# Kernel optimization log

Measured on AMD Instinct MI355X. Metric: run time of the kernel, lower is better.

The kernel has to match this reference:

```python
import jax, jax.numpy as jnp
import numpy as np

T_STEPS, B, I, H = 512, 64, 128, 256
LAST_K, RSIZE = 16, 32


def _xavier(key, shape):
    fan_out, fan_in = shape[0], shape[-1]
    std = (2.0 / (fan_in + fan_out)) ** 0.5
    return (std * jax.random.normal(key, shape)).astype(jnp.float32)


def setup_inputs() -> dict:
    key = jax.random.key(0)
    ks = jax.random.split(key, 8)
    inp = {"x": jax.random.normal(ks[0], (T_STEPS, B, I), dtype=jnp.float32)}
    for n, k in zip(["Wf", "Wi", "Wo", "Wg"], ks[1:5]):
        inp[n + "_w"] = _xavier(k, (H, H + I))
        inp[n + "_b"] = jnp.zeros((H,), jnp.float32)
    inp["Ua_w"] = _xavier(ks[5], (H, H))
    inp["Va_w"] = _xavier(ks[6], (H, H))
    inp["v"] = _xavier(ks[7], (1, H))
    return inp


def _forward(x, Wf_w, Wf_b, Wi_w, Wi_b, Wo_w, Wo_b, Wg_w, Wg_b, Ua_w, Va_w, v):
    T = x.shape[0]
    vv = v[0]  # [H]
    neg_inf = jnp.float32(-jnp.inf)

    def lstm(st, ct, xt):
        inp = jnp.concatenate([st, xt], axis=1)  # [B, H+I], order (hidden, input) as in torch cat((st, x), 1)
        ft = jax.nn.sigmoid(inp @ Wf_w.T + Wf_b)
        it = jax.nn.sigmoid(inp @ Wi_w.T + Wi_b)
        ot = jax.nn.sigmoid(inp @ Wo_w.T + Wo_b)
        gt = jnp.tanh(inp @ Wg_w.T + Wg_b)
        ct = ft * ct + it * gt
        return ot * jnp.tanh(ct), ct

    # ---- step 0 (reset path): st = zero hidden, no attention ----
    st0 = jnp.zeros((B, H), jnp.float32)
    h0, ct0 = lstm(st0, jnp.zeros((B, H), jnp.float32), x[0])
    mem0 = jnp.zeros((LAST_K, B, H), jnp.float32).at[-1].set(h0)  # ring of last_k hiddens (zeros = not yet filled)
    carry0 = (st0, ct0, mem0,
              jnp.zeros((RSIZE, B, H), jnp.float32),   # long_mem buckets
              jnp.full((RSIZE, B), neg_inf),            # long_mask (-inf = empty bucket)
              jnp.zeros((T, B), jnp.float32),           # long_scores (detached accumulator)
              jnp.zeros((B, RSIZE), jnp.float32),       # buck_scores
              jnp.zeros((B,), jnp.int32))               # per-sample bucket fill count

    def body(carry, tx):
        st, ct, mem, long_mem, long_mask, long_scores, buck, fill = carry
        t, xt = tx
        slots = jnp.arange(LAST_K)
        short_valid = slots >= (LAST_K - t)  # slot j holds h_{t-LAST_K+j}; valid iff time >= 0
        # ---- additive attention over short memory + long-term buckets ----
        q = st @ Va_w.T                              # [B,H]
        Uahs = mem @ Ua_w.T                          # [LAST_K,B,H]
        long_uas = long_mem @ Ua_w.T                 # [RSIZE,B,H]
        es = jnp.einsum('kbh,h->kb', jnp.tanh(q[None] + Uahs), vv)
        es = jnp.where(short_valid[:, None], es, neg_inf)
        es_long = jnp.einsum('rbh,h->rb', jnp.tanh(q[None] + long_uas), vv) + long_mask
        alphas = jax.nn.softmax(jnp.concatenate([es, es_long], 0), axis=0)  # [LAST_K+RSIZE,B]
        # accumulate detached attention mass onto absolute-time scores
        det_a = jax.lax.stop_gradient(alphas[:LAST_K])
        times = jnp.clip(t - LAST_K + slots, 0, T - 1)
        long_scores = long_scores.at[times].add(jnp.where(short_valid[:, None], det_a, 0.0))
        comb = jnp.concatenate([mem, long_mem], 0)   # [LAST_K+RSIZE,B,H]
        ct_att = jnp.einsum('nb,nbh->bh', alphas, comb)
        st = 0.5 * (mem[-1] + ct_att)                # comb_hs[-1-rsize] == previous hidden
        # ---- LSTM gating ----
        hidden, ct = lstm(st, ct, xt)
        # ---- bucket insert / argmin-replace (active once t >= LAST_K) ----
        cand = mem[0]                                # h_{t-LAST_K} == memory[0]
        cand_score = jax.lax.stop_gradient(
            jax.lax.dynamic_index_in_dim(long_scores, jnp.clip(t - LAST_K, 0, T - 1), 0, keepdims=False))  # [B]
        minp = jnp.argmin(buck, axis=1)              # [B], first-min like torch.argmin
        min_val = jnp.take_along_axis(buck, minp[:, None], axis=1)[:, 0]
        full = fill >= RSIZE
        addpos = jnp.where(full, minp, fill)
        do_upd = (t >= LAST_K) & (jnp.logical_not(full) | (cand_score > min_val))
        onehot = (jnp.arange(RSIZE)[None, :] == addpos[:, None]) & do_upd[:, None]  # [B,RSIZE]
        sel = onehot.T                               # [RSIZE,B]
        long_mem = jnp.where(sel[:, :, None], cand[None], long_mem)
        long_mask = jnp.where(sel, 0.0, long_mask)
        buck = jnp.where(onehot, cand_score[:, None], buck)
        fill = fill + (do_upd & jnp.logical_not(full)).astype(jnp.int32)
        # ---- push hidden into short-memory ring ----
        mem = jnp.concatenate([mem[1:], hidden[None]], 0)
        return (st, ct, mem, long_mem, long_mask, long_scores, buck, fill), hidden

    ts = jnp.arange(1, T)
    _, hs = jax.lax.scan(jax.checkpoint(body), carry0, (ts, x[1:]))
    return jnp.concatenate([h0[None], hs], 0)  # [T,B,H]


def reference(x, Wf_w, Wf_b, Wi_w, Wi_b, Wo_w, Wo_b, Wg_w, Wg_b, Ua_w, Va_w, v):
    return _forward(x, Wf_w, Wf_b, Wi_w, Wi_b, Wo_w, Wo_b, Wg_w, Wg_b, Ua_w, Va_w, v)
```

## Files before the change

kernel.cpp:

```cpp
#include <hip/hip_runtime.h>
#include <hip/hip_fp16.h>

#define T_STEPS 512
#define NB      64
#define NI      128
#define NH      256
#define LK      16
#define RS      32
#define NS      (LK + RS)

#define WP_OFF   0
#define VAP8_OFF 786432
#define UAP8_OFF 917504
#define GX_OFF   5242880
#define WS_NEED  (GX_OFF + (size_t)T_STEPS * NB * NH * 8)

typedef _Float16 half2v __attribute__((ext_vector_type(2)));

#if defined(__has_builtin)
# if __has_builtin(__builtin_amdgcn_make_buffer_rsrc) && \
     __has_builtin(__builtin_amdgcn_raw_buffer_load_b128) && \
     __has_builtin(__builtin_amdgcn_raw_buffer_load_b64)
#  define USE_BUFLD 1
# endif
#endif
#ifndef USE_BUFLD
# define USE_BUFLD 0
#endif

template <typename D, typename S>
__device__ __forceinline__ D bcastv(S s) {
    static_assert(sizeof(D) == sizeof(S), "size mismatch");
    D d; __builtin_memcpy(&d, &s, sizeof(D)); return d;
}

#if USE_BUFLD
#define DECL_RSRC(name, ptr) \
    auto name = __builtin_amdgcn_make_buffer_rsrc((void*)(ptr), (short)0, -1, 0x00020000)
#define LD16(name, ptr, idx) \
    bcastv<uint4>(__builtin_amdgcn_raw_buffer_load_b128(name, (int)((idx) * 16), 0, 1))
#define LD8(name, ptr, idx) \
    bcastv<uint2>(__builtin_amdgcn_raw_buffer_load_b64(name, (int)((idx) * 8), 0, 1))
#else
#define DECL_RSRC(name, ptr) int name = 0; (void)name
#define LD16(name, ptr, idx) ((ptr)[idx])
#define LD8(name, ptr, idx)  ((ptr)[idx])
#endif

__device__ __forceinline__ float hdot(unsigned int w, unsigned int s, float c) {
    return __builtin_amdgcn_fdot2(__builtin_bit_cast(half2v, w),
                                  __builtin_bit_cast(half2v, s), c, false);
}

__device__ __forceinline__ float fsig(float x) {
    return __builtin_amdgcn_rcpf(1.0f + __expf(-x));
}
__device__ __forceinline__ float ftanh(float x) {
    x = fminf(15.0f, fmaxf(-15.0f, x));
    float e = __expf(2.0f * x);
    return (e - 1.0f) * __builtin_amdgcn_rcpf(e + 1.0f);
}

__global__ void prep_weights(const float* __restrict__ Wf, const float* __restrict__ Wi,
                             const float* __restrict__ Wo, const float* __restrict__ Wg,
                             const float* __restrict__ Ua, const float* __restrict__ Va,
                             unsigned char* __restrict__ ws) {
    int e = blockIdx.x * 256 + threadIdx.x;
    if (e < 49152) {
        int h = e & 255, k2 = e >> 8, k = 2 * k2;
        uint4 w; __half2 t;
        t = __floats2half2_rn(Wf[h * 384 + k], Wf[h * 384 + k + 1]); w.x = *(unsigned int*)&t;
        t = __floats2half2_rn(Wi[h * 384 + k], Wi[h * 384 + k + 1]); w.y = *(unsigned int*)&t;
        t = __floats2half2_rn(Wo[h * 384 + k], Wo[h * 384 + k + 1]); w.z = *(unsigned int*)&t;
        t = __floats2half2_rn(Wg[h * 384 + k], Wg[h * 384 + k + 1]); w.w = *(unsigned int*)&t;
        ((uint4*)(ws + WP_OFF))[e] = w;
    } else {
        int e2 = e - 49152;
        const float* S = (e2 < 8192) ? Va : Ua;
        int e3 = e2 & 8191;
        int h = e3 & 255, j = e3 >> 8, k = 8 * j;
        uint4 w; __half2 t;
        t = __floats2half2_rn(S[h * 256 + k + 0], S[h * 256 + k + 1]); w.x = *(unsigned int*)&t;
        t = __floats2half2_rn(S[h * 256 + k + 2], S[h * 256 + k + 3]); w.y = *(unsigned int*)&t;
        t = __floats2half2_rn(S[h * 256 + k + 4], S[h * 256 + k + 5]); w.z = *(unsigned int*)&t;
        t = __floats2half2_rn(S[h * 256 + k + 6], S[h * 256 + k + 7]); w.w = *(unsigned int*)&t;
        ((uint4*)(ws + VAP8_OFF))[e2] = w;
    }
}

__global__ __launch_bounds__(256) void gx_gemm(const float* __restrict__ x,
                                               unsigned char* __restrict__ ws) {
    const int t = blockIdx.x, bg = blockIdx.y, tid = threadIdx.x;
    const uint4* __restrict__ WP = (const uint4*)(ws + WP_OFF);
    uint2* __restrict__ GX = (uint2*)(ws + GX_OFF);
    __shared__ float s_xx[16 * 128];
    const float* xb = x + ((size_t)t * NB + bg * 16) * NI;
#pragma unroll
    for (int r = 0; r < 8; ++r) s_xx[tid + 256 * r] = xb[tid + 256 * r];
    __syncthreads();
    const int h = tid;
    float acc[16][4];
#pragma unroll
    for (int bb = 0; bb < 16; ++bb) { acc[bb][0] = acc[bb][1] = acc[bb][2] = acc[bb][3] = 0.f; }
    for (int k2 = 128; k2 < 192; ++k2) {
        uint4 w = WP[k2 * NH + h];
        float2 wf = __half22float2(*(const __half2*)&w.x);
        float2 wi = __half22float2(*(const __half2*)&w.y);
        float2 wo = __half22float2(*(const __half2*)&w.z);
        float2 wg = __half22float2(*(const __half2*)&w.w);
        int kk = 2 * k2 - 256;
#pragma unroll
        for (int bb = 0; bb < 16; ++bb) {
            float2 xv = *(const float2*)(s_xx + bb * 128 + kk);
            acc[bb][0] += wf.x * xv.x + wf.y * xv.y;
            acc[bb][1] += wi.x * xv.x + wi.y * xv.y;
            acc[bb][2] += wo.x * xv.x + wo.y * xv.y;
            acc[bb][3] += wg.x * xv.x + wg.y * xv.y;
        }
    }
#pragma unroll
    for (int bb = 0; bb < 16; ++bb) {
        __half2 p0 = __floats2half2_rn(acc[bb][0], acc[bb][1]);
        __half2 p1 = __floats2half2_rn(acc[bb][2], acc[bb][3]);
        uint2 u; u.x = *(unsigned int*)&p0; u.y = *(unsigned int*)&p1;
        GX[((size_t)t * NB + bg * 16 + bb) * NH + h] = u;
    }
}

template <int USE_GX>
__global__ __launch_bounds__(1024, 1) void rel_lstm(
    const float* __restrict__ x,
    const float* __restrict__ bf_g, const float* __restrict__ bi_g,
    const float* __restrict__ bo_g, const float* __restrict__ bg_g,
    const float* __restrict__ vv_g,
    unsigned char* __restrict__ ws, float* __restrict__ out) {
    const int tid = threadIdx.x;
    const int b   = blockIdx.x;
    const int wv  = tid >> 6;
    const int ln  = tid & 63;
    const int h16 = (wv << 4) | (ln & 15);
    const int kc  = ln >> 4;

    const uint4* __restrict__ WP   = (const uint4*)(ws + WP_OFF);
    const uint4* __restrict__ VaP8 = (const uint4*)(ws + VAP8_OFF);
    const uint2* __restrict__ GX   = (const uint2*)(ws + GX_OFF);
    DECL_RSRC(rWP, ws + WP_OFF);
    DECL_RSRC(rVU, ws + VAP8_OFF);
    DECL_RSRC(rGX, ws + GX_OFF);

    __shared__ __align__(16) _Float16 s_in_h[NH + NI];
    __shared__ __align__(16) _Float16 s_hid_h[NH];
    __shared__ __align__(16) float s_q[NH];
    __shared__ __align__(16) float s_v[NH];
    __shared__ __align__(16) float s_mem[LK][NH];
    __shared__ __align__(16) float s_memua[LK][NH + 8];
    __shared__ __align__(16) float s_lraw[RS * NH];
    __shared__ __align__(16) float s_lua[RS * NH];
    __shared__ float s_es[NS], s_al[NS];
    __shared__ float s_scores[T_STEPS];
    __shared__ float s_mask[RS], s_buck[RS];
    __shared__ float s_minv;
    __shared__ int s_minp, s_fill, s_upd, s_pos;

    for (int i = tid; i < LK * NH; i += 1024) ((float*)s_mem)[i] = 0.f;
    for (int i = tid; i < LK * (NH + 8); i += 1024) ((float*)s_memua)[i] = 0.f;
    for (int i = tid; i < RS * NH; i += 1024) { s_lraw[i] = 0.f; s_lua[i] = 0.f; }
    if (tid < T_STEPS) s_scores[tid] = 0.f;
    if (tid < NH) s_v[tid] = vv_g[tid];
    if (tid < (NH + NI) / 2) ((unsigned int*)s_in_h)[tid] = 0u;
    if (tid < RS) { s_mask[tid] = -1e30f; s_buck[tid] = 0.f; }
    if (tid == 0) { s_fill = 0; s_upd = 0; s_pos = 0; s_minv = 0.f; s_minp = 0; }
    float bfv = 0.f, biv = 0.f, bov = 0.f, bgv = 0.f;
    if (kc == 0) { bfv = bf_g[h16]; biv = bi_g[h16]; bov = bo_g[h16]; bgv = bg_g[h16]; }
    if (!USE_GX && tid < 64) {
        float2 xv = ((const float2*)(x + (size_t)b * NI))[tid];
        __half2 hx = __floats2half2_rn(xv.x, xv.y);
        ((unsigned int*)s_in_h)[NH / 2 + tid] = *(unsigned int*)&hx;
    }
    float ct = 0.f;
    int base = 0;
    __syncthreads();

    for (int t = 0; t < T_STEPS; ++t) {
        float evA = 0.f, evB = 0.f;
        uint2 gx = {0u, 0u};
        if (USE_GX && kc == 0) gx = LD8(rGX, GX, ((size_t)t * NB + b) * NH + h16);
        if (t > 0) {
            {
                const int pofs = (wv < 8) ? 0 : 8192;
                const uint4* SRC = (wv < 8) ? (const uint4*)s_in_h : (const uint4*)s_hid_h;
                const int hh = ((wv & 7) << 5) | (ln & 31);
                const int ch = ln >> 5;
                float acc = 0.f;
#pragma unroll 8
                for (int jj = 0; jj < 16; ++jj) {
                    int j = (ch << 4) | jj;
                    uint4 w = LD16(rVU, VaP8, (j << 8) + hh + pofs);
                    uint4 s = SRC[j];
                    acc = hdot(w.x, s.x, acc);
                    acc = hdot(w.y, s.y, acc);
                    acc = hdot(w.z, s.z, acc);
                    acc = hdot(w.w, s.w, acc);
                }
                acc += __shfl_xor(acc, 32, 64);
                if (ch == 0) {
                    if (wv < 8) s_q[hh] = acc;
                    else        s_memua[(base + LK - 1) & (LK - 1)][hh] = acc;
                }
                if (kc == 1) {
                    int p0 = base & (LK - 1);
                    evA = s_mem[p0][h16];
                    evB = s_memua[p0][h16];
                }
                if (!USE_GX && tid < 64) {
                    float2 xv = ((const float2*)(x + ((size_t)t * NB + b) * NI))[tid];
                    __half2 hx = __floats2half2_rn(xv.x, xv.y);
                    ((unsigned int*)s_in_h)[NH / 2 + tid] = *(unsigned int*)&hx;
                }
            }
            __syncthreads();
            if (tid < 768) {
                const int row = tid >> 4, l = tid & 15;
                bool skip;
                const float* ua;
                if (row < LK) { skip = row < LK - t; ua = s_memua[(base + row) & (LK - 1)]; }
                else          { skip = s_mask[row - LK] < -1e29f; ua = s_lua + (row - LK) * NH; }
                float esv = -1e30f;
                if (!skip) {
                    float p = 0.f;
#pragma unroll
                    for (int jj = 0; jj < 4; ++jj) {
                        int hh = (l << 2) + (jj << 6);
                        float4 q4 = *(const float4*)(s_q + hh);
                        float4 v4 = *(const float4*)(s_v + hh);
                        float4 u4 = *(const float4*)(ua + hh);
                        p += v4.x * ftanh(q4.x + u4.x);
                        p += v4.y * ftanh(q4.y + u4.y);
                        p += v4.z * ftanh(q4.z + u4.z);
                        p += v4.w * ftanh(q4.w + u4.w);
                    }
                    p += __shfl_xor(p, 1, 16);
                    p += __shfl_xor(p, 2, 16);
                    p += __shfl_xor(p, 4, 16);
                    p += __shfl_xor(p, 8, 16);
                    esv = p;
                }
                if (l == 0) s_es[row] = esv;
            } else if (tid >= 960 && tid < 992) {
                int l = tid - 960;
                float v = s_buck[l]; int idx = l;
#pragma unroll
                for (int off = 1; off < 32; off <<= 1) {
                    float v2 = __shfl_xor(v, off, 32);
                    int  i2 = __shfl_xor(idx, off, 32);
                    if (v2 < v || (v2 == v && i2 < idx)) { v = v2; idx = i2; }
                }
                if (l == 0) { s_minv = v; s_minp = idx; }
            }
            __syncthreads();
            if (tid < 64) {
                float e = (tid < NS) ? s_es[tid] : -1e30f;
                float m = e;
#pragma unroll
                for (int off = 32; off; off >>= 1) m = fmaxf(m, __shfl_xor(m, off, 64));
                float a = (tid < NS) ? __expf(e - m) : 0.f;
                float ssum = a;
#pragma unroll
                for (int off = 32; off; off >>= 1) ssum += __shfl_xor(ssum, off, 64);
                float al = a * __builtin_amdgcn_rcpf(ssum);
                if (tid < NS) s_al[tid] = al;
                float cs = 0.f;
                if (tid < LK) {
                    int time = t - LK + tid;
                    if (time >= 0) {
                        float ns = s_scores[time] + al;
                        s_scores[time] = ns;
                        cs = ns;
                    }
                }
                if (tid == 0) {
                    int upd = 0, pos = 0;
                    if (t >= LK) {
                        int fill = s_fill;
                        bool full = fill >= RS;
                        upd = (!full) || (cs > s_minv);
                        pos = full ? s_minp : fill;
                        if (upd) { s_mask[pos] = 0.f; s_buck[pos] = cs; if (!full) s_fill = fill + 1; }
                    }
                    s_upd = upd; s_pos = pos;
                }
            }
            __syncthreads();
            {
                float catt = 0.f;
                const int n0 = kc * 12;
#pragma unroll
                for (int n = n0; n < n0 + 12; ++n) {
                    float a = s_al[n];
                    if (n < LK) catt += a * s_mem[(base + n) & (LK - 1)][h16];
                    else if (a != 0.f) catt += a * s_lraw[(n - LK) * NH + h16];
                }
                catt += __shfl_xor(catt, 16, 64);
                catt += __shfl_xor(catt, 32, 64);
                if (kc == 0) {
                    float stv = 0.5f * (s_mem[(base + LK - 1) & (LK - 1)][h16] + catt);
                    s_in_h[h16] = (_Float16)stv;
                }
            }
            __syncthreads();
        }
        {
            constexpr int KP = USE_GX ? 32 : 48;
            const unsigned int* S2 = (const unsigned int*)s_in_h;
            float af = 0.f, ai = 0.f, ao = 0.f, ag = 0.f;
            const int lo = kc * KP;
#pragma unroll 8
            for (int k2 = lo; k2 < lo + KP; ++k2) {
                uint4 w = LD16(rWP, WP, (k2 << 8) + h16);
                unsigned int s2 = S2[k2];
                af = hdot(w.x, s2, af);
                ai = hdot(w.y, s2, ai);
                ao = hdot(w.z, s2, ao);
                ag = hdot(w.w, s2, ag);
            }
            af += __shfl_xor(af, 16, 64); af += __shfl_xor(af, 32, 64);
            ai += __shfl_xor(ai, 16, 64); ai += __shfl_xor(ai, 32, 64);
            ao += __shfl_xor(ao, 16, 64); ao += __shfl_xor(ao, 32, 64);
            ag += __shfl_xor(ag, 16, 64); ag += __shfl_xor(ag, 32, 64);
            if (kc == 0) {
                float pf = af + bfv, pi = ai + biv, po = ao + bov, pg = ag + bgv;
                if (USE_GX) {
                    float2 fi = __half22float2(*(const __half2*)&gx.x);
                    float2 og = __half22float2(*(const __half2*)&gx.y);
                    pf += fi.x; pi += fi.y; po += og.x; pg += og.y;
                }
                float f  = fsig(pf);
                float ii = fsig(pi);
                float o  = fsig(po);
                float g  = ftanh(pg);
                ct = f * ct + ii * g;
                float hid = o * ftanh(ct);
                out[((size_t)t * NB + b) * NH + h16] = hid;
                s_mem[base & (LK - 1)][h16] = hid;
                s_hid_h[h16] = (_Float16)hid;
            } else if (kc == 1 && s_upd) {
                s_lraw[s_pos * NH + h16] = evA;
                s_lua[s_pos * NH + h16]  = evB;
            }
        }
        base++;
        __syncthreads();
    }
}

extern "C" void kernel_launch(void* const* d_in, const int* in_sizes, int n_in,
                              void* d_out, int out_size, void* d_ws, size_t ws_size,
                              hipStream_t stream) {
    const float* x  = (const float*)d_in[0];
    const float* Wf = (const float*)d_in[1];
    const float* bf = (const float*)d_in[2];
    const float* Wi = (const float*)d_in[3];
    const float* bi = (const float*)d_in[4];
    const float* Wo = (const float*)d_in[5];
    const float* bo = (const float*)d_in[6];
    const float* Wg = (const float*)d_in[7];
    const float* bg = (const float*)d_in[8];
    const float* Ua = (const float*)d_in[9];
    const float* Va = (const float*)d_in[10];
    const float* vv = (const float*)d_in[11];
    unsigned char* ws = (unsigned char*)d_ws;
    float* out = (float*)d_out;

    prep_weights<<<256, 256, 0, stream>>>(Wf, Wi, Wo, Wg, Ua, Va, ws);
    if (ws_size >= WS_NEED) {
        gx_gemm<<<dim3(T_STEPS, 4), 256, 0, stream>>>(x, ws);
        rel_lstm<1><<<NB, 1024, 0, stream>>>(x, bf, bi, bo, bg, vv, ws, out);
    } else {
        rel_lstm<0><<<NB, 1024, 0, stream>>>(x, bf, bi, bo, bg, vv, ws, out);
    }
}
```

Before: 5.057 ms.

## Overlap attention projections with score phase and remove one barrier per step

```diff
diff --git a/kernel.cpp b/kernel.cpp
--- a/kernel.cpp
+++ b/kernel.cpp
@@ -5,6 +5,7 @@
 #define NB      64
 #define NI      128
 #define NH      256
+#define NHP     264
 #define LK      16
 #define RS      32
 #define NS      (LK + RS)
@@ -152,21 +153,20 @@
     __shared__ __align__(16) _Float16 s_hid_h[NH];
     __shared__ __align__(16) float s_q[NH];
     __shared__ __align__(16) float s_v[NH];
-    __shared__ __align__(16) float s_mem[LK][NH];
-    __shared__ __align__(16) float s_memua[LK][NH + 8];
-    __shared__ __align__(16) float s_lraw[RS * NH];
-    __shared__ __align__(16) float s_lua[RS * NH];
+    __shared__ __align__(16) float s_mem[LK][NHP];
+    __shared__ __align__(16) float s_memua[LK][NHP];
+    __shared__ __align__(16) float s_lraw[RS * NHP];
+    __shared__ __align__(16) float s_lua[RS * NHP];
     __shared__ float s_es[NS], s_al[NS];
     __shared__ float s_scores[T_STEPS];
     __shared__ float s_mask[RS], s_buck[RS];
     __shared__ float s_minv;
     __shared__ int s_minp, s_fill, s_upd, s_pos;
 
-    for (int i = tid; i < LK * NH; i += 1024) ((float*)s_mem)[i] = 0.f;
-    for (int i = tid; i < LK * (NH + 8); i += 1024) ((float*)s_memua)[i] = 0.f;
-    for (int i = tid; i < RS * NH; i += 1024) { s_lraw[i] = 0.f; s_lua[i] = 0.f; }
+    for (int i = tid; i < LK * NHP; i += 1024) { ((float*)s_mem)[i] = 0.f; ((float*)s_memua)[i] = 0.f; }
+    for (int i = tid; i < RS * NHP; i += 1024) { s_lraw[i] = 0.f; s_lua[i] = 0.f; }
     if (tid < T_STEPS) s_scores[tid] = 0.f;
-    if (tid < NH) s_v[tid] = vv_g[tid];
+    if (tid < NH) { s_v[tid] = vv_g[tid]; s_q[tid] = 0.f; }
     if (tid < (NH + NI) / 2) ((unsigned int*)s_in_h)[tid] = 0u;
     if (tid < RS) { s_mask[tid] = -1e30f; s_buck[tid] = 0.f; }
     if (tid == 0) { s_fill = 0; s_upd = 0; s_pos = 0; s_minv = 0.f; s_minp = 0; }
@@ -186,47 +186,71 @@
         uint2 gx = {0u, 0u};
         if (USE_GX && kc == 0) gx = LD8(rGX, GX, ((size_t)t * NB + b) * NH + h16);
         if (t > 0) {
-            {
-                const int pofs = (wv < 8) ? 0 : 8192;
-                const uint4* SRC = (wv < 8) ? (const uint4*)s_in_h : (const uint4*)s_hid_h;
-                const int hh = ((wv & 7) << 5) | (ln & 31);
-                const int ch = ln >> 5;
-                float acc = 0.f;
+            if (tid < 768) {
+                const int row = tid >> 4, l = tid & 15;
+                if (row != LK - 1) {
+                    bool skip;
+                    const float* ua;
+                    if (row < LK) { skip = row < LK - t; ua = s_memua[(base + row) & (LK - 1)]; }
+                    else          { skip = s_mask[row - LK] < -1e29f; ua = s_lua + (row - LK) * NHP; }
+                    float esv = -1e30f;
+                    if (!skip) {
+                        float p = 0.f;
+#pragma unroll
+                        for (int jj = 0; jj < 4; ++jj) {
+                            int hh = (l << 2) + (jj << 6);
+                            float4 q4 = *(const float4*)(s_q + hh);
+                            float4 v4 = *(const float4*)(s_v + hh);
+                            float4 u4 = *(const float4*)(ua + hh);
+                            p += v4.x * ftanh(q4.x + u4.x);
+                            p += v4.y * ftanh(q4.y + u4.y);
+                            p += v4.z * ftanh(q4.z + u4.z);
+                            p += v4.w * ftanh(q4.w + u4.w);
+                        }
+                        p += __shfl_xor(p, 1, 16);
+                        p += __shfl_xor(p, 2, 16);
+                        p += __shfl_xor(p, 4, 16);
+                        p += __shfl_xor(p, 8, 16);
+                        esv = p;
+                    }
+                    if (l == 0) s_es[row] = esv;
+                } else {
+                    float v = s_buck[l]; int idx = l;
+                    float v2 = s_buck[l + 16];
+                    if (v2 < v) { v = v2; idx = l + 16; }
+#pragma unroll
+                    for (int off = 1; off < 16; off <<= 1) {
+                        float vv2 = __shfl_xor(v, off, 16);
+                        int  ii2 = __shfl_xor(idx, off, 16);
+                        if (vv2 < v || (vv2 == v && ii2 < idx)) { v = vv2; idx = ii2; }
+                    }
+                    if (l == 0) { s_minv = v; s_minp = idx; }
+                }
+            } else {
+                const int h = ((wv - 12) << 6) | ln;
+                const uint4* SRC = (const uint4*)s_hid_h;
+                float accA = 0.f, accB = 0.f;
 #pragma unroll 8
-                for (int jj = 0; jj < 16; ++jj) {
-                    int j = (ch << 4) | jj;
-                    uint4 w = LD16(rVU, VaP8, (j << 8) + hh + pofs);
+                for (int j = 0; j < 16; ++j) {
+                    uint4 w = LD16(rVU, VaP8, (j << 8) + h + 8192);
                     uint4 s = SRC[j];
-                    acc = hdot(w.x, s.x, acc);
-                    acc = hdot(w.y, s.y, acc);
-                    acc = hdot(w.z, s.z, acc);
-                    acc = hdot(w.w, s.w, acc);
-                }
-                acc += __shfl_xor(acc, 32, 64);
-                if (ch == 0) {
-                    if (wv < 8) s_q[hh] = acc;
-                    else        s_memua[(base + LK - 1) & (LK - 1)][hh] = acc;
-                }
-                if (kc == 1) {
-                    int p0 = base & (LK - 1);
-                    evA = s_mem[p0][h16];
-                    evB = s_memua[p0][h16];
-                }
-                if (!USE_GX && tid < 64) {
-                    float2 xv = ((const float2*)(x + ((size_t)t * NB + b) * NI))[tid];
-                    __half2 hx = __floats2half2_rn(xv.x, xv.y);
-                    ((unsigned int*)s_in_h)[NH / 2 + tid] = *(unsigned int*)&hx;
-                }
+                    accA = hdot(w.x, s.x, accA); accA = hdot(w.y, s.y, accA);
+                    accA = hdot(w.z, s.z, accA); accA = hdot(w.w, s.w, accA);
+                }
+#pragma unroll 8
+                for (int j = 16; j < 32; ++j) {
+                    uint4 w = LD16(rVU, VaP8, (j << 8) + h + 8192);
+                    uint4 s = SRC[j];
+                    accB = hdot(w.x, s.x, accB); accB = hdot(w.y, s.y, accB);
+                    accB = hdot(w.z, s.z, accB); accB = hdot(w.w, s.w, accB);
+                }
+                s_memua[(base + LK - 1) & (LK - 1)][h] = accA + accB;
             }
             __syncthreads();
-            if (tid < 768) {
-                const int row = tid >> 4, l = tid & 15;
-                bool skip;
-                const float* ua;
-                if (row < LK) { skip = row < LK - t; ua = s_memua[(base + row) & (LK - 1)]; }
-                else          { skip = s_mask[row - LK] < -1e29f; ua = s_lua + (row - LK) * NH; }
-                float esv = -1e30f;
-                if (!skip) {
+            if (tid < 64) {
+                if (tid < 16) {
+                    const int l = tid;
+                    const float* ua = s_memua[(base + LK - 1) & (LK - 1)];
                     float p = 0.f;
 #pragma unroll
                     for (int jj = 0; jj < 4; ++jj) {
@@ -243,22 +267,8 @@
                     p += __shfl_xor(p, 2, 16);
                     p += __shfl_xor(p, 4, 16);
                     p += __shfl_xor(p, 8, 16);
-                    esv = p;
-                }
-                if (l == 0) s_es[row] = esv;
-            } else if (tid >= 960 && tid < 992) {
-                int l = tid - 960;
-                float v = s_buck[l]; int idx = l;
-#pragma unroll
-                for (int off = 1; off < 32; off <<= 1) {
-                    float v2 = __shfl_xor(v, off, 32);
-                    int  i2 = __shfl_xor(idx, off, 32);
-                    if (v2 < v || (v2 == v && i2 < idx)) { v = v2; idx = i2; }
-                }
-                if (l == 0) { s_minv = v; s_minp = idx; }
-            }
-            __syncthreads();
-            if (tid < 64) {
+                    if (l == 0) s_es[LK - 1] = p;
+                }
                 float e = (tid < NS) ? s_es[tid] : -1e30f;
                 float m = e;
 #pragma unroll
@@ -298,13 +308,22 @@
                 for (int n = n0; n < n0 + 12; ++n) {
                     float a = s_al[n];
                     if (n < LK) catt += a * s_mem[(base + n) & (LK - 1)][h16];
-                    else if (a != 0.f) catt += a * s_lraw[(n - LK) * NH + h16];
+                    else if (a != 0.f) catt += a * s_lraw[(n - LK) * NHP + h16];
                 }
                 catt += __shfl_xor(catt, 16, 64);
                 catt += __shfl_xor(catt, 32, 64);
                 if (kc == 0) {
                     float stv = 0.5f * (s_mem[(base + LK - 1) & (LK - 1)][h16] + catt);
                     s_in_h[h16] = (_Float16)stv;
+                } else if (kc == 1) {
+                    int p0 = base & (LK - 1);
+                    evA = s_mem[p0][h16];
+                    evB = s_memua[p0][h16];
+                }
+                if (!USE_GX && tid < 64) {
+                    float2 xv = ((const float2*)(x + ((size_t)t * NB + b) * NI))[tid];
+                    __half2 hx = __floats2half2_rn(xv.x, xv.y);
+                    ((unsigned int*)s_in_h)[NH / 2 + tid] = *(unsigned int*)&hx;
                 }
             }
             __syncthreads();
@@ -343,9 +362,29 @@
                 out[((size_t)t * NB + b) * NH + h16] = hid;
                 s_mem[base & (LK - 1)][h16] = hid;
                 s_hid_h[h16] = (_Float16)hid;
-            } else if (kc == 1 && s_upd) {
-                s_lraw[s_pos * NH + h16] = evA;
-                s_lua[s_pos * NH + h16]  = evB;
+            } else if (kc == 1) {
+                if (t > 0 && s_upd) {
+                    s_lraw[s_pos * NHP + h16] = evA;
+                    s_lua[s_pos * NHP + h16]  = evB;
+                }
+            } else if (kc == 2) {
+                const uint4* SRC = (const uint4*)s_in_h;
+                float accA = 0.f, accB = 0.f;
+#pragma unroll 8
+                for (int j = 0; j < 16; ++j) {
+                    uint4 w = LD16(rVU, VaP8, (j << 8) + h16);
+                    uint4 s = SRC[j];
+                    accA = hdot(w.x, s.x, accA); accA = hdot(w.y, s.y, accA);
+                    accA = hdot(w.z, s.z, accA); accA = hdot(w.w, s.w, accA);
+                }
+#pragma unroll 8
+                for (int j = 16; j < 32; ++j) {
+                    uint4 w = LD16(rVU, VaP8, (j << 8) + h16);
+                    uint4 s = SRC[j];
+                    accB = hdot(w.x, s.x, accB); accB = hdot(w.y, s.y, accB);
+                    accB = hdot(w.z, s.z, accB); accB = hdot(w.w, s.w, accB);
+                }
+                s_q[h16] = accA + accB;
             }
         }
         base++;
```

Measured after the change: 7.997 ms. 1.58x slower.

## Move query projection to previous step's tail and pad shared memory rows

Applied to the files above, without the earlier changes.

```diff
diff --git a/kernel.cpp b/kernel.cpp
--- a/kernel.cpp
+++ b/kernel.cpp
@@ -5,6 +5,7 @@
 #define NB      64
 #define NI      128
 #define NH      256
+#define NHP     260
 #define LK      16
 #define RS      32
 #define NS      (LK + RS)
@@ -152,21 +153,21 @@
     __shared__ __align__(16) _Float16 s_hid_h[NH];
     __shared__ __align__(16) float s_q[NH];
     __shared__ __align__(16) float s_v[NH];
-    __shared__ __align__(16) float s_mem[LK][NH];
+    __shared__ __align__(16) float s_mem[LK][NHP];
     __shared__ __align__(16) float s_memua[LK][NH + 8];
-    __shared__ __align__(16) float s_lraw[RS * NH];
-    __shared__ __align__(16) float s_lua[RS * NH];
+    __shared__ __align__(16) float s_lraw[RS * NHP];
+    __shared__ __align__(16) float s_lua[RS * NHP];
     __shared__ float s_es[NS], s_al[NS];
     __shared__ float s_scores[T_STEPS];
     __shared__ float s_mask[RS], s_buck[RS];
     __shared__ float s_minv;
     __shared__ int s_minp, s_fill, s_upd, s_pos;
 
-    for (int i = tid; i < LK * NH; i += 1024) ((float*)s_mem)[i] = 0.f;
+    for (int i = tid; i < LK * NHP; i += 1024) ((float*)s_mem)[i] = 0.f;
     for (int i = tid; i < LK * (NH + 8); i += 1024) ((float*)s_memua)[i] = 0.f;
-    for (int i = tid; i < RS * NH; i += 1024) { s_lraw[i] = 0.f; s_lua[i] = 0.f; }
+    for (int i = tid; i < RS * NHP; i += 1024) { s_lraw[i] = 0.f; s_lua[i] = 0.f; }
     if (tid < T_STEPS) s_scores[tid] = 0.f;
-    if (tid < NH) s_v[tid] = vv_g[tid];
+    if (tid < NH) { s_v[tid] = vv_g[tid]; s_q[tid] = 0.f; }
     if (tid < (NH + NI) / 2) ((unsigned int*)s_in_h)[tid] = 0u;
     if (tid < RS) { s_mask[tid] = -1e30f; s_buck[tid] = 0.f; }
     if (tid == 0) { s_fill = 0; s_upd = 0; s_pos = 0; s_minv = 0.f; s_minp = 0; }
@@ -187,25 +188,23 @@
         if (USE_GX && kc == 0) gx = LD8(rGX, GX, ((size_t)t * NB + b) * NH + h16);
         if (t > 0) {
             {
-                const int pofs = (wv < 8) ? 0 : 8192;
-                const uint4* SRC = (wv < 8) ? (const uint4*)s_in_h : (const uint4*)s_hid_h;
-                const int hh = ((wv & 7) << 5) | (ln & 31);
-                const int ch = ln >> 5;
-                float acc = 0.f;
+                if (wv >= 8) {
+                    const uint4* SRC = (const uint4*)s_hid_h;
+                    const int hh = ((wv & 7) << 5) | (ln & 31);
+                    const int ch = ln >> 5;
+                    float acc = 0.f;
 #pragma unroll 8
-                for (int jj = 0; jj < 16; ++jj) {
-                    int j = (ch << 4) | jj;
-                    uint4 w = LD16(rVU, VaP8, (j << 8) + hh + pofs);
-                    uint4 s = SRC[j];
-                    acc = hdot(w.x, s.x, acc);
-                    acc = hdot(w.y, s.y, acc);
-                    acc = hdot(w.z, s.z, acc);
-                    acc = hdot(w.w, s.w, acc);
-                }
-                acc += __shfl_xor(acc, 32, 64);
-                if (ch == 0) {
-                    if (wv < 8) s_q[hh] = acc;
-                    else        s_memua[(base + LK - 1) & (LK - 1)][hh] = acc;
+                    for (int jj = 0; jj < 16; ++jj) {
+                        int j = (ch << 4) | jj;
+                        uint4 w = LD16(rVU, VaP8, (j << 8) + hh + 8192);
+                        uint4 s = SRC[j];
+                        acc = hdot(w.x, s.x, acc);
+                        acc = hdot(w.y, s.y, acc);
+                        acc = hdot(w.z, s.z, acc);
+                        acc = hdot(w.w, s.w, acc);
+                    }
+                    acc += __shfl_xor(acc, 32, 64);
+                    if (ch == 0) s_memua[(base + LK - 1) & (LK - 1)][hh] = acc;
                 }
                 if (kc == 1) {
                     int p0 = base & (LK - 1);
@@ -224,7 +223,7 @@
                 bool skip;
                 const float* ua;
                 if (row < LK) { skip = row < LK - t; ua = s_memua[(base + row) & (LK - 1)]; }
-                else          { skip = s_mask[row - LK] < -1e29f; ua = s_lua + (row - LK) * NH; }
+                else          { skip = s_mask[row - LK] < -1e29f; ua = s_lua + (row - LK) * NHP; }
                 float esv = -1e30f;
                 if (!skip) {
                     float p = 0.f;
@@ -298,7 +297,7 @@
                 for (int n = n0; n < n0 + 12; ++n) {
                     float a = s_al[n];
                     if (n < LK) catt += a * s_mem[(base + n) & (LK - 1)][h16];
-                    else if (a != 0.f) catt += a * s_lraw[(n - LK) * NH + h16];
+                    else if (a != 0.f) catt += a * s_lraw[(n - LK) * NHP + h16];
                 }
                 catt += __shfl_xor(catt, 16, 64);
                 catt += __shfl_xor(catt, 32, 64);
@@ -343,9 +342,29 @@
                 out[((size_t)t * NB + b) * NH + h16] = hid;
                 s_mem[base & (LK - 1)][h16] = hid;
                 s_hid_h[h16] = (_Float16)hid;
-            } else if (kc == 1 && s_upd) {
-                s_lraw[s_pos * NH + h16] = evA;
-                s_lua[s_pos * NH + h16]  = evB;
+            } else if (kc == 1 && t > 0 && s_upd) {
+                s_lraw[s_pos * NHP + h16] = evA;
+                s_lua[s_pos * NHP + h16]  = evB;
+            }
+            if (wv < 4) {
+                const int hq = (wv << 6) | ln;
+                const uint4* SRC = (const uint4*)s_in_h;
+                float accA = 0.f, accB = 0.f;
+#pragma unroll 8
+                for (int j = 0; j < 16; ++j) {
+                    uint4 w = LD16(rVU, VaP8, (j << 8) + hq);
+                    uint4 s = SRC[j];
+                    accA = hdot(w.x, s.x, accA); accA = hdot(w.y, s.y, accA);
+                    accA = hdot(w.z, s.z, accA); accA = hdot(w.w, s.w, accA);
+                }
+#pragma unroll 8
+                for (int j = 16; j < 32; ++j) {
+                    uint4 w = LD16(rVU, VaP8, (j << 8) + hq);
+                    uint4 s = SRC[j];
+                    accB = hdot(w.x, s.x, accB); accB = hdot(w.y, s.y, accB);
+                    accB = hdot(w.z, s.z, accB); accB = hdot(w.w, s.w, accB);
+                }
+                s_q[hq] = accA + accB;
             }
         }
         base++;
```

Measured after the change: 6.118 ms. +21.0%, slower.
